# Kernel optimization log

Measured on AMD Instinct MI355X. Metric: run time of the kernel, lower is better.

Reference implementation:

```python
import jax, jax.numpy as jnp
import numpy as np
import math

N_NODES = 4096
NUM_FEATURES = 500
NHID = 256
RATIO = 0.75


def _build_adj(x):
    # Faithful vectorization of get_threshold/get_edge_index:
    # t = 0.5 * max_{i,j} ||x_i - x_j||^2 ; directed edges (src=i -> dst=j) for j>i with d2<t.
    # Dense adjacency A[dst, src] (jit-friendly; edge count is data-dependent in the original).
    sq = jnp.sum(x * x, axis=1)
    d2 = sq[:, None] + sq[None, :] - 2.0 * (x @ x.T)  # [N,N] squared distances
    t = 0.5 * jnp.max(d2)
    N = x.shape[0]
    lower = jnp.tril(jnp.ones((N, N), dtype=bool), k=-1)  # entry [j,i], j>i
    return jnp.where(lower & (d2 < t), 1.0, 0.0).astype(x.dtype)


def _gcn(A, x, W, b):
    # PyG GCNConv: add self-loops, symmetric normalization D^-1/2 (A+I) D^-1/2, then @ (xW) + b
    N = A.shape[0]
    Ah = A + jnp.eye(N, dtype=A.dtype)
    dis = jax.lax.rsqrt(jnp.sum(Ah, axis=1))  # deg >= 1 due to self loops
    norm = (dis[:, None] * Ah) * dis[None, :]
    return norm @ (x @ W) + b


def _sag_pool(A, x, Wr, Wn, bn, k):
    # SAGPooling with default GraphConv scorer: score = sum-aggr(neighbors)@Wn + bn + x@Wr
    score = jnp.tanh(((A @ x) @ Wn + bn + x @ Wr)[:, 0])  # [N]
    vals, perm = jax.lax.top_k(score, k)  # top ceil(ratio*N) nodes, descending
    xp = x[perm] * vals[:, None]
    Ap = A[perm][:, perm]  # filter edges to surviving nodes
    return Ap, xp


def _readout(x):
    # single graph (batch=None -> all zeros): [gmp, gap] -> [1, 2*nhid]
    return jnp.concatenate([jnp.max(x, axis=0), jnp.mean(x, axis=0)])[None, :]


def setup_inputs() -> dict:
    key = jax.random.key(0)
    ks = jax.random.split(key, 16)
    s = 0.02
    inp = {
        "feature": jax.random.normal(ks[0], (N_NODES, NUM_FEATURES), jnp.float32),
        "img_info": jax.random.normal(ks[1], (N_NODES, 6), jnp.float32),
        "W_pos": jax.random.normal(ks[2], (6, 12), jnp.float32) * s,
        "b_pos": jnp.zeros((12,), jnp.float32),
        "W1": jax.random.normal(ks[3], (512, NHID), jnp.float32) * s,
        "b1": jnp.zeros((NHID,), jnp.float32),
        "W2": jax.random.normal(ks[4], (NHID, NHID), jnp.float32) * s,
        "b2": jnp.zeros((NHID,), jnp.float32),
        "W3": jax.random.normal(ks[5], (NHID, NHID), jnp.float32) * s,
        "b3": jnp.zeros((NHID,), jnp.float32),
        "Wr1": jax.random.normal(ks[6], (NHID, 1), jnp.float32) * s,
        "Wn1": jax.random.normal(ks[7], (NHID, 1), jnp.float32) * s,
        "bs1": jnp.zeros((1,), jnp.float32),
        "Wr2": jax.random.normal(ks[8], (NHID, 1), jnp.float32) * s,
        "Wn2": jax.random.normal(ks[9], (NHID, 1), jnp.float32) * s,
        "bs2": jnp.zeros((1,), jnp.float32),
        "Wr3": jax.random.normal(ks[10], (NHID, 1), jnp.float32) * s,
        "Wn3": jax.random.normal(ks[11], (NHID, 1), jnp.float32) * s,
        "bs3": jnp.zeros((1,), jnp.float32),
    }
    return inp


def reference(feature, img_info, W_pos, b_pos, W1, b1, W2, b2, W3, b3,
              Wr1, Wn1, bs1, Wr2, Wn2, bs2, Wr3, Wn3, bs3):
    pos = jax.nn.relu(img_info @ W_pos + b_pos)          # [N,12]
    feat = jnp.concatenate([feature, pos], axis=1)       # [N,512]
    N = feat.shape[0]
    k1 = math.ceil(RATIO * N)
    k2 = math.ceil(RATIO * k1)
    k3 = math.ceil(RATIO * k2)

    A = _build_adj(feat)

    x = jax.nn.relu(_gcn(A, feat, W1, b1))
    A, x = _sag_pool(A, x, Wr1, Wn1, bs1, k1)
    x1 = _readout(x)

    x = jax.nn.relu(_gcn(A, x, W2, b2))
    A, x = _sag_pool(A, x, Wr2, Wn2, bs2, k2)
    x2 = _readout(x)

    x = jax.nn.relu(_gcn(A, x, W3, b3))
    A, x = _sag_pool(A, x, Wr3, Wn3, bs3, k3)
    x3 = _readout(x)

    return x1 + x2 + x3  # [1, 2*NHID]
```

## Files before the change

### kernel.cpp

```cpp
#include <hip/hip_runtime.h>
#include <hip/hip_bf16.h>
#include <math.h>

typedef __hip_bfloat16 bf16;
typedef unsigned short ushort;
typedef unsigned int uint;
typedef unsigned long long ull;
static __device__ __forceinline__ float b2f(bf16 x){ return __bfloat162float(x); }

static __device__ __forceinline__ float ldf(const void* p, int i, int isbf){
    return isbf ? b2f(((const bf16*)p)[i]) : ((const float*)p)[i];
}
static __device__ __forceinline__ ushort f2b(float x){
    return __bfloat16_as_ushort(__float2bfloat16(x));
}
static __device__ __forceinline__ uint fcode(float v){
    uint u = __float_as_uint(v);
    return (u & 0x80000000u) ? ~u : (u | 0x80000000u);
}
static __device__ __forceinline__ float fdecode(uint c){
    uint u = (c & 0x80000000u) ? (c & 0x7FFFFFFFu) : ~c;
    return __uint_as_float(u);
}

#define NN    4096
#define FEAT0 500
#define DIN   512
#define NH    256
#define KL1   3072
#define KL2   2304
#define KL3   1728
#define EDGE_CAP 786432u
#define NTRI  2080

typedef __attribute__((ext_vector_type(8)))  short v8s;
typedef __attribute__((ext_vector_type(16))) float v16f;

static __device__ __forceinline__ void gl_lds16(const ushort* g, ushort* l){
    __builtin_amdgcn_global_load_lds(
        (const __attribute__((address_space(1))) void*)g,
        (__attribute__((address_space(3))) void*)l, 16, 0, 0);
}

static __device__ __forceinline__ void detect_bf16(const void* p, int n, int t,
        uint* flag){
    if (t < 256 && t < n){
        uint e = ((uint)((const ushort*)p)[t] >> 7) & 0xFFu;
        if (e >= 135u) atomicAnd(flag, 0u);
    }
}

struct DtIn { const void* p[19]; int n[19]; };
__global__ __launch_bounds__(512) void k_prep(DtIn da,
        ushort* __restrict__ Xb, float* __restrict__ sq, ushort* __restrict__ Wb,
        unsigned* __restrict__ dflag, float* __restrict__ degA,
        uint* __restrict__ maxU, float* __restrict__ sums,
        unsigned* __restrict__ ecnt, unsigned* __restrict__ maxd2,
        float* __restrict__ tmin){
    int row = blockIdx.x, t = threadIdx.x;
    if (row < NN){
        __shared__ uint fl[4];
        if (t < 4) fl[t] = 1u;
        __syncthreads();
        detect_bf16(da.p[0], da.n[0], t, &fl[0]);
        detect_bf16(da.p[1], da.n[1], t, &fl[1]);
        detect_bf16(da.p[2], da.n[2], t, &fl[2]);
        detect_bf16(da.p[3], da.n[3], t, &fl[3]);
        __syncthreads();
        int f_feat = (int)fl[0], f_img = (int)fl[1], f_wp = (int)fl[2], f_bp = (int)fl[3];
        float v;
        if (t < FEAT0) v = ldf(da.p[0], row*FEAT0 + t, f_feat);
        else {
            int c = t - FEAT0;
            float acc = ldf(da.p[3], c, f_bp);
            #pragma unroll
            for (int d = 0; d < 6; d++)
                acc += ldf(da.p[1], row*6+d, f_img) * ldf(da.p[2], d*12+c, f_wp);
            v = fmaxf(acc, 0.f);
        }
        bf16 vb = __float2bfloat16(v);
        Xb[row*DIN + t] = __bfloat16_as_ushort(vb);
        float vr = b2f(vb);
        float vsq = vr*vr;
        #pragma unroll
        for (int off = 32; off >= 1; off >>= 1) vsq += __shfl_down(vsq, off);
        __shared__ float red[8];
        if ((t & 63) == 0) red[t >> 6] = vsq;
        __syncthreads();
        if (t == 0){
            float sres = 0.f;
            #pragma unroll
            for (int i = 0; i < 8; i++) sres += red[i];
            sq[row] = sres;
        }
    } else if (row < NN + 64){
        __shared__ uint fl[3];
        if (t < 3) fl[t] = 1u;
        __syncthreads();
        detect_bf16(da.p[4], da.n[4], t, &fl[0]);
        detect_bf16(da.p[6], da.n[6], t, &fl[1]);
        detect_bf16(da.p[8], da.n[8], t, &fl[2]);
        __syncthreads();
        int i0 = ((row - NN)*512 + t)*8;
        #pragma unroll
        for (int j = 0; j < 8; j++){
            int idx = i0 + j;
            float v;
            if (idx < 131072)       v = ldf(da.p[4], idx,          (int)fl[0]);
            else if (idx < 196608)  v = ldf(da.p[6], idx - 131072, (int)fl[1]);
            else                    v = ldf(da.p[8], idx - 196608, (int)fl[2]);
            Wb[idx] = __bfloat16_as_ushort(__float2bfloat16(v));
        }
    } else {
        __shared__ uint fl19[19];
        if (t < 19) fl19[t] = 1u;
        for (int i = t; i < NN; i += 512) degA[i] = 1.0f;
        for (int i = t; i < 4096; i += 512) tmin[i] = INFINITY;
        for (int i = t; i < 768; i += 512){ maxU[i] = 0x007FFFFFu; sums[i] = 0.f; }
        if (t == 0){
            #pragma unroll
            for (int i = 0; i < 8; i++) ecnt[i] = 0u;
            maxd2[0] = 0u;
        }
        __syncthreads();
        for (int idx = t; idx < 19*256; idx += 512){
            int i = idx >> 8, j = idx & 255;
            if (j < da.n[i]){
                uint e = ((uint)((const ushort*)da.p[i])[j] >> 7) & 0xFFu;
                if (e >= 135u) atomicAnd(&fl19[i], 0u);
            }
        }
        __syncthreads();
        if (t < 19) dflag[t] = fl19[t];
    }
}

static __device__ __forceinline__ v16f mm_tile(const ushort* __restrict__ Arows,
        const ushort* __restrict__ Brows, int K, ushort* As, ushort* Bs,
        int tid, int wv, int l31, int hi){
    int lane = tid & 63;
    int ro = lane >> 3, cch = lane & 7;
    int r0 = wv*16 + ro, r1 = wv*16 + 8 + ro;
    const ushort* gA0 = Arows + (size_t)r0*K + ((cch ^ (r0&7))<<3);
    const ushort* gA1 = Arows + (size_t)r1*K + ((cch ^ (r1&7))<<3);
    const ushort* gB0 = Brows + (size_t)r0*K + ((cch ^ (r0&7))<<3);
    const ushort* gB1 = Brows + (size_t)r1*K + ((cch ^ (r1&7))<<3);
    ushort* lA0 = As + (wv*16)*64;
    ushort* lA1 = As + (wv*16+8)*64;
    ushort* lB0 = Bs + (wv*16)*64;
    ushort* lB1 = Bs + (wv*16+8)*64;
    int wwr = wv >> 1, wwc = wv & 1;
    int ra0 = (wwr*32 + l31)*64, rbp = (wwc*32 + l31)*64;
    int fr7a = (wwr*32 + l31) & 7, fr7b = (wwc*32 + l31) & 7;
    v16f acc = {};
    int NC = K >> 6;
    for (int c = 0; c < NC; c++){
        int k0 = c*64;
        __syncthreads();
        gl_lds16(gA0 + k0, lA0);
        gl_lds16(gA1 + k0, lA1);
        gl_lds16(gB0 + k0, lB0);
        gl_lds16(gB1 + k0, lB1);
        __syncthreads();
        #pragma unroll
        for (int ks = 0; ks < 4; ks++){
            int gq = ks*2 + hi;
            v8s a = *(const v8s*)&As[ra0 + ((gq^fr7a)<<3)];
            v8s b = *(const v8s*)&Bs[rbp + ((gq^fr7b)<<3)];
            acc = __builtin_amdgcn_mfma_f32_32x32x16_bf16(a, b, acc, 0, 0, 0);
        }
    }
    return acc;
}

static __device__ __forceinline__ void xw_body(const ushort* __restrict__ Ab,
        const ushort* __restrict__ Wb, float* __restrict__ XW, int rb, int cb,
        int K, ushort* As, ushort* Bs){
    int tid = threadIdx.x, lane = tid & 63, wv = tid >> 6;
    int wwr = wv >> 1, wwc = wv & 1;
    int l31 = lane & 31, hi = lane >> 5;
    int arow0 = tid >> 3, ag = tid & 7;
    int arow1 = arow0 + 32;
    int da0 = arow0*64 + ((ag^(arow0&7))<<3);
    int da1 = arow1*64 + ((ag^(arow1&7))<<3);
    const size_t baseA = (size_t)rb*64*K;
    int kr = tid >> 2, ng = tid & 3;
    float4 a0p = *(const float4*)(Ab + baseA + (size_t)arow0*K + ag*8);
    float4 a1p = *(const float4*)(Ab + baseA + (size_t)arow1*K + ag*8);
    float4 b0p = *(const float4*)(Wb + (size_t)kr*NH + cb*64 + ng*16);
    float4 b1p = *(const float4*)(Wb + (size_t)kr*NH + cb*64 + ng*16 + 8);
    v16f acc = {};
    int ra0 = (wwr*32 + l31)*64, rbp = (wwc*32 + l31)*64;
    int fr7a = (wwr*32 + l31) & 7, fr7b = (wwc*32 + l31) & 7;
    int kg = kr >> 3, k7 = kr & 7;
    int NC = K >> 6;
    for (int c = 0; c < NC; c++){
        __syncthreads();
        *(float4*)&As[da0] = a0p; *(float4*)&As[da1] = a1p;
        const ushort* bw0 = (const ushort*)&b0p;
        const ushort* bw1 = (const ushort*)&b1p;
        #pragma unroll
        for (int j = 0; j < 8; j++){
            int nn = ng*16 + j;
            Bs[nn*64 + ((kg^(nn&7))<<3) + k7] = bw0[j];
        }
        #pragma unroll
        for (int j = 0; j < 8; j++){
            int nn = ng*16 + 8 + j;
            Bs[nn*64 + ((kg^(nn&7))<<3) + k7] = bw1[j];
        }
        __syncthreads();
        if (c + 1 < NC){
            int k0 = (c+1)*64;
            a0p = *(const float4*)(Ab + baseA + (size_t)arow0*K + k0 + ag*8);
            a1p = *(const float4*)(Ab + baseA + (size_t)arow1*K + k0 + ag*8);
            b0p = *(const float4*)(Wb + (size_t)(k0+kr)*NH + cb*64 + ng*16);
            b1p = *(const float4*)(Wb + (size_t)(k0+kr)*NH + cb*64 + ng*16 + 8);
        }
        #pragma unroll
        for (int ks = 0; ks < 4; ks++){
            int gq = ks*2 + hi;
            v8s a = *(const v8s*)&As[ra0 + ((gq^fr7a)<<3)];
            v8s b = *(const v8s*)&Bs[rbp + ((gq^fr7b)<<3)];
            acc = __builtin_amdgcn_mfma_f32_32x32x16_bf16(a, b, acc, 0, 0, 0);
        }
    }
    int n  = cb*64 + wwc*32 + l31;
    int mb = rb*64 + wwr*32 + 4*hi;
    #pragma unroll
    for (int i = 0; i < 16; i++){
        int m = mb + (i&3) + 8*(i>>2);
        XW[(size_t)m*NH + n] = acc[i];
    }
}

template<int PASS>
__global__ __launch_bounds__(256) void k_gram(const ushort* __restrict__ Xb,
        const float* __restrict__ sq, unsigned* __restrict__ maxd2,
        float* __restrict__ tmin, unsigned* __restrict__ ecnt,
        unsigned* __restrict__ edges, float* __restrict__ deg,
        const ushort* __restrict__ Wb, float* __restrict__ XW){
    __shared__ __align__(16) ushort As[64*64];
    __shared__ __align__(16) ushort Bs[64*64];
    int b = blockIdx.x;
    if (PASS == 1){
        if (b < 256){
            xw_body(Xb, Wb, XW, b >> 2, b & 3, DIN, As, Bs);
            return;
        }
        b -= 256;
    }
    float ff = sqrtf(8.f*(float)b + 1.f);
    int rb = (int)((ff - 1.f) * 0.5f);
    while ((rb+1)*(rb+2)/2 <= b) rb++;
    while (rb*(rb+1)/2 > b) rb--;
    int cb = b - rb*(rb+1)/2;

    int tid = threadIdx.x;
    float tthr = 0.f;
    if (PASS == 2){
        tthr = 0.5f * __uint_as_float(maxd2[0]);
        if (tmin[rb*64 + cb] >= tthr) return;
    }
    int lane = tid & 63, wv = tid >> 6;
    int l31 = lane & 31, hi = lane >> 5;
    int wwr = wv >> 1, wwc = wv & 1;
    v16f acc = mm_tile(Xb + (size_t)rb*64*DIN, Xb + (size_t)cb*64*DIN, DIN,
                       As, Bs, tid, wv, l31, hi);
    int rbase = rb*64 + wwr*32 + 4*hi;
    int col   = cb*64 + wwc*32 + l31;
    float sqc = sq[col];
    if (PASS == 1){
        float m = 0.f, mn = INFINITY;
        #pragma unroll
        for (int i = 0; i < 16; i++){
            int r = rbase + (i&3) + 8*(i>>2);
            float d2 = sq[r] + sqc - 2.f*acc[i];
            if (r != col) m = fmaxf(m, d2);
            if (r > col)  mn = fminf(mn, d2);
        }
        #pragma unroll
        for (int off = 32; off >= 1; off >>= 1){
            m  = fmaxf(m,  __shfl_down(m,  off));
            mn = fminf(mn, __shfl_down(mn, off));
        }
        __shared__ float wmax[4], wmin[4];
        if (lane == 0){ wmax[wv] = m; wmin[wv] = mn; }
        __syncthreads();
        if (tid == 0){
            float mm = fmaxf(fmaxf(wmax[0], wmax[1]), fmaxf(wmax[2], wmax[3]));
            tmin[rb*64 + cb] = fminf(fminf(wmin[0], wmin[1]), fminf(wmin[2], wmin[3]));
            atomicMax(maxd2, __float_as_uint(fmaxf(mm, 0.f)));
        }
    } else {
        #pragma unroll
        for (int i = 0; i < 16; i++){
            int r = rbase + (i&3) + 8*(i>>2);
            float d2 = sq[r] + sqc - 2.f*acc[i];
            if (r > col && d2 < tthr){
                unsigned idx = atomicAdd(ecnt, 1u);
                if (idx < EDGE_CAP){
                    edges[idx] = ((unsigned)r << 16) | (unsigned)col;
                    atomicAdd(&deg[r], 1.0f);
                }
            }
        }
    }
}

__global__ __launch_bounds__(256) void k_xwp(const float* __restrict__ Xn,
        const int* __restrict__ perm, const float* __restrict__ svals,
        const ushort* __restrict__ Wb, float* __restrict__ XW, int M,
        uint* __restrict__ maxU, float* __restrict__ sums, int layer){
    int rb = blockIdx.x, cb = blockIdx.y;
    __shared__ __align__(16) ushort As[64*64];
    __shared__ __align__(16) ushort Bs[64*64];
    __shared__ float pmx[256], psm[256];
    int tid = threadIdx.x, lane = tid & 63, wv = tid >> 6;
    int wwr = wv >> 1, wwc = wv & 1;
    int l31 = lane & 31, hi = lane >> 5;
    int arow0 = tid >> 3, ag = tid & 7;
    int arow1 = arow0 + 32;
    int da0 = arow0*64 + ((ag^(arow0&7))<<3);
    int da1 = arow1*64 + ((ag^(arow1&7))<<3);
    int p0 = perm[rb*64 + arow0]; float sv0 = svals[rb*64 + arow0];
    int p1 = perm[rb*64 + arow1]; float sv1 = svals[rb*64 + arow1];
    int kr = tid >> 2, ng = tid & 3;
    int kg = kr >> 3, k7 = kr & 7;
    int ra0 = (wwr*32 + l31)*64, rbp = (wwc*32 + l31)*64;
    int fr7a = (wwr*32 + l31) & 7, fr7b = (wwc*32 + l31) & 7;

    float4 xa0 = *(const float4*)(Xn + (size_t)p0*NH + ag*8);
    float4 xa1 = *(const float4*)(Xn + (size_t)p0*NH + ag*8 + 4);
    float4 xb0 = *(const float4*)(Xn + (size_t)p1*NH + ag*8);
    float4 xb1 = *(const float4*)(Xn + (size_t)p1*NH + ag*8 + 4);
    float4 wb0 = *(const float4*)(Wb + (size_t)kr*NH + cb*64 + ng*16);
    float4 wb1 = *(const float4*)(Wb + (size_t)kr*NH + cb*64 + ng*16 + 8);

    v16f acc = {};
    for (int c = 0; c < 4; c++){
        __syncthreads();
        {
            __align__(16) ushort ta[8];
            ta[0]=f2b(xa0.x*sv0); ta[1]=f2b(xa0.y*sv0); ta[2]=f2b(xa0.z*sv0); ta[3]=f2b(xa0.w*sv0);
            ta[4]=f2b(xa1.x*sv0); ta[5]=f2b(xa1.y*sv0); ta[6]=f2b(xa1.z*sv0); ta[7]=f2b(xa1.w*sv0);
            *(float4*)&As[da0] = *(const float4*)ta;
            __align__(16) ushort tb[8];
            tb[0]=f2b(xb0.x*sv1); tb[1]=f2b(xb0.y*sv1); tb[2]=f2b(xb0.z*sv1); tb[3]=f2b(xb0.w*sv1);
            tb[4]=f2b(xb1.x*sv1); tb[5]=f2b(xb1.y*sv1); tb[6]=f2b(xb1.z*sv1); tb[7]=f2b(xb1.w*sv1);
            *(float4*)&As[da1] = *(const float4*)tb;
        }
        {
            const ushort* bw0 = (const ushort*)&wb0;
            const ushort* bw1 = (const ushort*)&wb1;
            #pragma unroll
            for (int j = 0; j < 8; j++){
                int nn = ng*16 + j;
                Bs[nn*64 + ((kg^(nn&7))<<3) + k7] = bw0[j];
            }
            #pragma unroll
            for (int j = 0; j < 8; j++){
                int nn = ng*16 + 8 + j;
                Bs[nn*64 + ((kg^(nn&7))<<3) + k7] = bw1[j];
            }
        }
        __syncthreads();
        if (c < 3){
            int k0 = (c+1)*64;
            xa0 = *(const float4*)(Xn + (size_t)p0*NH + k0 + ag*8);
            xa1 = *(const float4*)(Xn + (size_t)p0*NH + k0 + ag*8 + 4);
            xb0 = *(const float4*)(Xn + (size_t)p1*NH + k0 + ag*8);
            xb1 = *(const float4*)(Xn + (size_t)p1*NH + k0 + ag*8 + 4);
            wb0 = *(const float4*)(Wb + (size_t)(k0+kr)*NH + cb*64 + ng*16);
            wb1 = *(const float4*)(Wb + (size_t)(k0+kr)*NH + cb*64 + ng*16 + 8);
        }
        if (cb == 0){
            int cc = tid & 63, q = tid >> 6;
            int gg = cc >> 3, c7 = cc & 7;
            float m = -INFINITY, s = 0.f;
            #pragma unroll
            for (int i = 0; i < 16; i++){
                int rr = q*16 + i;
                float v = __uint_as_float(((uint)As[rr*64 + ((gg^(rr&7))<<3) + c7]) << 16);
                m = fmaxf(m, v); s += v;
            }
            pmx[tid] = m; psm[tid] = s;
            __syncthreads();
            if (tid < 64){
                float mm = fmaxf(fmaxf(pmx[tid], pmx[tid+64]), fmaxf(pmx[tid+128], pmx[tid+192]));
                float ss = psm[tid] + psm[tid+64] + psm[tid+128] + psm[tid+192];
                atomicMax(&maxU[layer*NH + c*64 + tid], fcode(mm));
                atomicAdd(&sums[layer*NH + c*64 + tid], ss);
            }
        }
        #pragma unroll
        for (int ks = 0; ks < 4; ks++){
            int gq = ks*2 + hi;
            v8s a = *(const v8s*)&As[ra0 + ((gq^fr7a)<<3)];
            v8s b = *(const v8s*)&Bs[rbp + ((gq^fr7b)<<3)];
            acc = __builtin_amdgcn_mfma_f32_32x32x16_bf16(a, b, acc, 0, 0, 0);
        }
    }
    int n  = cb*64 + wwc*32 + l31;
    int mb = rb*64 + wwr*32 + 4*hi;
    #pragma unroll
    for (int i = 0; i < 16; i++){
        int m = mb + (i&3) + 8*(i>>2);
        XW[(size_t)m*NH + n] = acc[i];
    }
}

__global__ __launch_bounds__(256) void k_gcnscore(const float* __restrict__ XW,
        const unsigned* __restrict__ edges, const unsigned* __restrict__ ecnt, int slot,
        const float* __restrict__ deg, const void* __restrict__ b,
        const void* __restrict__ Wn, const void* __restrict__ Wr, const void* __restrict__ bs,
        const unsigned* __restrict__ fb, const unsigned* __restrict__ fWn,
        const unsigned* __restrict__ fWr, const unsigned* __restrict__ fbs,
        float* __restrict__ Xn, float* __restrict__ s1, float* __restrict__ z){
    int row = blockIdx.x, t = threadIdx.x;
    __shared__ unsigned eL[256];
    __shared__ unsigned Esh;
    if (t == 0){ unsigned E0 = ecnt[slot]; Esh = (E0 > EDGE_CAP) ? EDGE_CAP : E0; }
    __syncthreads();
    unsigned E = Esh;
    float disr = 1.0f / sqrtf(deg[row]);
    float acc = disr * XW[row*NH + t];
    for (unsigned base = 0; base < E; base += 256){
        unsigned nchunk = E - base; if (nchunk > 256) nchunk = 256;
        __syncthreads();
        if (t < nchunk) eL[t] = edges[base + t];
        __syncthreads();
        for (unsigned j = 0; j < nchunk; j++){
            unsigned ed = eL[j];
            if ((int)(ed >> 16) == row){
                int src = ed & 0xFFFFu;
                acc += (1.0f / sqrtf(deg[src])) * XW[src*NH + t];
            }
        }
    }
    float xn = fmaxf(fmaf(disr, acc, ldf(b, t, (int)fb[0])), 0.f);
    Xn[row*NH + t] = xn;
    float a  = xn * ldf(Wn, t, (int)fWn[0]);
    float bb = xn * ldf(Wr, t, (int)fWr[0]);
    for (int off = 32; off >= 1; off >>= 1){ a += __shfl_down(a, off); bb += __shfl_down(bb, off); }
    __shared__ float ra[4], rbv[4];
    int w = t >> 6;
    if ((t & 63) == 0){ ra[w] = a; rbv[w] = bb; }
    __syncthreads();
    if (t == 0){
        s1[row] = ra[0]+ra[1]+ra[2]+ra[3];
        z[row]  = rbv[0]+rbv[1]+rbv[2]+rbv[3] + ldf(bs, 0, (int)fbs[0]);
    }
}

static __device__ __forceinline__ uint2 radix_scan(const uint* hist, uint* wt,
        uint* ws, uint* sh, int t, int lane, int wv, uint kk, int NB){
    uint loc = 0;
    int b0 = t << 2;
    if (b0 < NB) loc = hist[b0] + hist[b0+1] + hist[b0+2] + hist[b0+3];
    uint s = loc;
    #pragma unroll
    for (int off = 1; off < 64; off <<= 1){
        uint u = __shfl_down(s, off);
        if (lane + off < 64) s += u;
    }
    if (lane == 0) wt[wv] = s;
    __syncthreads();
    if (t < 16){
        uint a = 0;
        for (int j = t + 1; j < 16; j++) a += wt[j];
        ws[t] = a;
    }
    __syncthreads();
    if (b0 < NB){
        uint run = ws[wv] + (s - loc);
        for (int b = b0 + 3; b >= b0; b--){
            uint h = hist[b];
            if (run < kk && run + h >= kk){ sh[0] = (uint)b; sh[1] = run; }
            run += h;
        }
    }
    __syncthreads();
    return make_uint2(sh[0], sh[1]);
}

__global__ __launch_bounds__(1024) void k_select(const float* __restrict__ z,
        const float* __restrict__ s1, int N, int k,
        const unsigned* __restrict__ eIn, unsigned* __restrict__ ecnt, int slotCur,
        unsigned* __restrict__ eOut, int slotOut,
        int* __restrict__ perm, float* __restrict__ svals,
        float* __restrict__ degN, int Nnext){
    __shared__ float zsh[4096];
    __shared__ int   rnk[4096];
    __shared__ uint  hist[4096];
    __shared__ uint  wcnt[16];
    __shared__ uint  wbase[16];
    __shared__ uint  sh[4];
    int t = threadIdx.x;
    int lane = t & 63, wv = t >> 6;
    for (int i = t; i < N; i += 1024){ zsh[i] = z[i]; rnk[i] = -1; }
    for (int i = t; i < Nnext; i += 1024) degN[i] = 1.0f;
    if (t == 0) sh[2] = 0u;
    __syncthreads();
    unsigned E = ecnt[slotCur]; if (E > EDGE_CAP) E = EDGE_CAP;
    for (unsigned e = t; e < E; e += 1024){
        unsigned ed = eIn[e];
        atomicAdd(&zsh[ed >> 16], s1[ed & 0xFFFFu]);
    }
    __syncthreads();
    bool v0 = t < N,        v1 = t+1024 < N,  v2 = t+2048 < N,  v3 = t+3072 < N;
    uint c0 = v0 ? fcode(zsh[t])      : 0u;
    uint c1 = v1 ? fcode(zsh[t+1024]) : 0u;
    uint c2 = v2 ? fcode(zsh[t+2048]) : 0u;
    uint c3 = v3 ? fcode(zsh[t+3072]) : 0u;

    for (int i = t; i < 4096; i += 1024) hist[i] = 0u;
    __syncthreads();
    if (v0){
        uint h0 = c0 >> 20, h1 = c1 >> 20, h2 = c2 >> 20, h3 = c3 >> 20;
        bool u1 = v1, u2 = v2, u3 = v3;
        uint n0 = 1;
        if (u1 && h1 == h0){ n0++; u1 = false; }
        if (u2 && h2 == h0){ n0++; u2 = false; }
        if (u3 && h3 == h0){ n0++; u3 = false; }
        atomicAdd(&hist[h0], n0);
        if (u1){
            uint n1 = 1;
            if (u2 && h2 == h1){ n1++; u2 = false; }
            if (u3 && h3 == h1){ n1++; u3 = false; }
            atomicAdd(&hist[h1], n1);
        }
        if (u2){
            uint n2 = 1;
            if (u3 && h3 == h2){ n2++; u3 = false; }
            atomicAdd(&hist[h2], n2);
        }
        if (u3) atomicAdd(&hist[h3], 1u);
    }
    __syncthreads();
    uint2 p1 = radix_scan(hist, wcnt, wbase, sh, t, lane, wv, (uint)k, 4096);
    uint B1 = p1.x; uint kk2 = (uint)k - p1.y;
    for (int i = t; i < 4096; i += 1024) hist[i] = 0u;
    __syncthreads();
    if (v0 && (c0 >> 20) == B1) atomicAdd(&hist[(c0 >> 8) & 0xFFFu], 1u);
    if (v1 && (c1 >> 20) == B1) atomicAdd(&hist[(c1 >> 8) & 0xFFFu], 1u);
    if (v2 && (c2 >> 20) == B1) atomicAdd(&hist[(c2 >> 8) & 0xFFFu], 1u);
    if (v3 && (c3 >> 20) == B1) atomicAdd(&hist[(c3 >> 8) & 0xFFFu], 1u);
    __syncthreads();
    uint2 p2 = radix_scan(hist, wcnt, wbase, sh, t, lane, wv, kk2, 4096);
    uint B2 = p2.x; uint kk3 = kk2 - p2.y;
    uint hi24 = (B1 << 12) | B2;
    for (int i = t; i < 256; i += 1024) hist[i] = 0u;
    __syncthreads();
    if (v0 && (c0 >> 8) == hi24) atomicAdd(&hist[c0 & 0xFFu], 1u);
    if (v1 && (c1 >> 8) == hi24) atomicAdd(&hist[c1 & 0xFFu], 1u);
    if (v2 && (c2 >> 8) == hi24) atomicAdd(&hist[c2 & 0xFFu], 1u);
    if (v3 && (c3 >> 8) == hi24) atomicAdd(&hist[c3 & 0xFFu], 1u);
    __syncthreads();
    uint2 p3 = radix_scan(hist, wcnt, wbase, sh, t, lane, wv, kk3, 256);
    uint T = (B1 << 20) | (B2 << 8) | p3.x;

    ull b0 = __ballot(v0 && c0 > T), b1 = __ballot(v1 && c1 > T);
    ull b2 = __ballot(v2 && c2 > T), b3 = __ballot(v3 && c3 > T);
    uint t0 = (uint)__popcll(b0), t1 = (uint)__popcll(b1);
    uint t2 = (uint)__popcll(b2), t3 = (uint)__popcll(b3);
    if (lane == 0) wcnt[wv] = t0 + t1 + t2 + t3;
    __syncthreads();
    if (t == 0){
        uint s = 0;
        for (int i = 0; i < 16; i++){ wbase[i] = s; s += wcnt[i]; }
        sh[1] = s;
    }
    __syncthreads();
    uint cntGT = sh[1];
    uint rem = (uint)k - cntGT;
    ull ltm = ((ull)1 << lane) - 1;
    uint off = wbase[wv];
    if (v0 && c0 > T){ uint r = off + (uint)__popcll(b0 & ltm); int i = t;
        perm[r] = i; svals[r] = tanhf(zsh[i]); rnk[i] = (int)r; }
    off += t0;
    if (v1 && c1 > T){ uint r = off + (uint)__popcll(b1 & ltm); int i = t+1024;
        perm[r] = i; svals[r] = tanhf(zsh[i]); rnk[i] = (int)r; }
    off += t1;
    if (v2 && c2 > T){ uint r = off + (uint)__popcll(b2 & ltm); int i = t+2048;
        perm[r] = i; svals[r] = tanhf(zsh[i]); rnk[i] = (int)r; }
    off += t2;
    if (v3 && c3 > T){ uint r = off + (uint)__popcll(b3 & ltm); int i = t+3072;
        perm[r] = i; svals[r] = tanhf(zsh[i]); rnk[i] = (int)r; }
    #pragma unroll
    for (int j = 0; j < 4; j++){
        int i = t + j*1024;
        bool vv = (j==0) ? v0 : (j==1) ? v1 : (j==2) ? v2 : v3;
        uint cc = (j==0) ? c0 : (j==1) ? c1 : (j==2) ? c2 : c3;
        if (vv && cc == T){
            uint e = atomicAdd(&sh[2], 1u);
            if (e < rem){
                uint r = cntGT + e;
                perm[r] = i; svals[r] = tanhf(zsh[i]); rnk[i] = (int)r;
            }
        }
    }
    __syncthreads();
    if (slotOut >= 0){
        for (unsigned e = t; e < E; e += 1024){
            unsigned ed = eIn[e];
            int nd = rnk[ed >> 16], ns = rnk[ed & 0xFFFFu];
            if (nd >= 0 && ns >= 0){
                unsigned idx = atomicAdd(&ecnt[slotOut], 1u);
                if (idx < EDGE_CAP){
                    eOut[idx] = ((unsigned)nd << 16) | (unsigned)ns;
                    atomicAdd(&degN[nd], 1.0f);
                }
            }
        }
    }
}

__global__ __launch_bounds__(256) void k_poolread3(const float* __restrict__ Xn,
        const int* __restrict__ perm, const float* __restrict__ svals, int k,
        uint* __restrict__ maxU, float* __restrict__ sums,
        unsigned* __restrict__ done, float* __restrict__ out){
    int b = blockIdx.x, t = threadIdx.x;
    float m = -INFINITY, s = 0.f;
    for (int r = b; r < k; r += 64){
        int p = perm[r];
        float v = Xn[p*NH + t] * svals[r];
        m = fmaxf(m, v); s += v;
    }
    atomicMax(&maxU[2*NH + t], fcode(m));
    atomicAdd(&sums[2*NH + t], s);
    __threadfence();
    __shared__ uint lastv;
    if (t == 0) lastv = atomicAdd(done, 1u);
    __syncthreads();
    if (lastv == 63u){
        uint m0 = atomicAdd(&maxU[t], 0u);
        uint m1 = atomicAdd(&maxU[NH + t], 0u);
        uint m2 = atomicAdd(&maxU[2*NH + t], 0u);
        float s0 = atomicAdd(&sums[t], 0.f);
        float s1v = atomicAdd(&sums[NH + t], 0.f);
        float s2 = atomicAdd(&sums[2*NH + t], 0.f);
        out[t] = fdecode(m0) + fdecode(m1) + fdecode(m2);
        out[NH + t] = s0*(1.0f/KL1) + s1v*(1.0f/KL2) + s2*(1.0f/KL3);
    }
}

extern "C" void kernel_launch(void* const* d_in, const int* in_sizes, int n_in,
                              void* d_out, int out_size, void* d_ws, size_t ws_size,
                              hipStream_t stream)
{
    const void* b1 = d_in[5];
    const void* b2 = d_in[7];
    const void* b3 = d_in[9];
    const void* Wr1 = d_in[10]; const void* Wn1 = d_in[11]; const void* bs1 = d_in[12];
    const void* Wr2 = d_in[13]; const void* Wn2 = d_in[14]; const void* bs2 = d_in[15];
    const void* Wr3 = d_in[16]; const void* Wn3 = d_in[17]; const void* bs3 = d_in[18];

    char* w = (char*)d_ws;
    auto alloc = [&](size_t bytes)->char*{ char* p = w; w += (bytes + 255) & ~(size_t)255; return p; };
    ushort*   Xb    = (ushort*)  alloc((size_t)NN*DIN*2);
    float*    Xn    = (float*)   alloc((size_t)NN*NH*4);
    float*    XW    = (float*)   alloc((size_t)NN*NH*4);
    ushort*   Wb    = (ushort*)  alloc((size_t)262144*2);
    unsigned* E0    = (unsigned*)alloc((size_t)EDGE_CAP*4);
    unsigned* E1    = (unsigned*)alloc((size_t)EDGE_CAP*4);
    float*    tmin  = (float*)   alloc(4096*4);
    float*    sq    = (float*)   alloc(NN*4);
    float*    degA  = (float*)   alloc(NN*4);
    float*    degB  = (float*)   alloc(NN*4);
    float*    s1    = (float*)   alloc(NN*4);
    float*    z     = (float*)   alloc(NN*4);
    int*      perm  = (int*)     alloc(NN*4);
    float*    svals = (float*)   alloc(NN*4);
    unsigned* ecnt  = (unsigned*)alloc(256);
    unsigned* maxd2 = (unsigned*)alloc(256);
    unsigned* dflag = (unsigned*)alloc(256);
    uint*     maxU  = (uint*)    alloc(768*4);
    float*    sums  = (float*)   alloc(768*4);
    (void)ws_size;

    DtIn da;
    for (int i = 0; i < 19; i++){ da.p[i] = d_in[i]; da.n[i] = in_sizes[i]; }

    k_prep<<<NN + 65, 512, 0, stream>>>(da, Xb, sq, Wb, dflag, degA, maxU, sums,
            ecnt, maxd2, tmin);
    k_gram<1><<<256 + NTRI, 256, 0, stream>>>(Xb, sq, maxd2, tmin, ecnt, E0, degA,
            Wb, XW);
    k_gram<2><<<NTRI, 256, 0, stream>>>(Xb, sq, maxd2, tmin, ecnt, E0, degA,
            Wb, XW);

    k_gcnscore<<<NN, 256, 0, stream>>>(XW, E0, ecnt, 0, degA, b1, Wn1, Wr1, bs1,
            dflag+5, dflag+11, dflag+10, dflag+12, Xn, s1, z);
    k_select<<<1, 1024, 0, stream>>>(z, s1, NN, KL1, E0, ecnt, 0, E1, 1,
            perm, svals, degB, KL1);

    k_xwp<<<dim3(48,4), 256, 0, stream>>>(Xn, perm, svals, Wb + 131072, XW, KL1,
            maxU, sums, 0);
    k_gcnscore<<<KL1, 256, 0, stream>>>(XW, E1, ecnt, 1, degB, b2, Wn2, Wr2, bs2,
            dflag+7, dflag+14, dflag+13, dflag+15, Xn, s1, z);
    k_select<<<1, 1024, 0, stream>>>(z, s1, KL1, KL2, E1, ecnt, 1, E0, 2,
            perm, svals, degA, KL2);

    k_xwp<<<dim3(36,4), 256, 0, stream>>>(Xn, perm, svals, Wb + 196608, XW, KL2,
            maxU, sums, 1);
    k_gcnscore<<<KL2, 256, 0, stream>>>(XW, E0, ecnt, 2, degA, b3, Wn3, Wr3, bs3,
            dflag+9, dflag+17, dflag+16, dflag+18, Xn, s1, z);
    k_select<<<1, 1024, 0, stream>>>(z, s1, KL2, KL3, E0, ecnt, 2,
            (unsigned*)nullptr, -1, perm, svals, degB, 0);
    k_poolread3<<<64, 256, 0, stream>>>(Xn, perm, svals, KL3, maxU, sums,
            ecnt + 3, (float*)d_out);
}
```

Before: 231.5 us.

## Enlarge Gram-matrix tiles to 128x128 with 512-thread blocks

The pairwise-distance Gram kernels now use 128x128 triangular tiles computed by 8 waves, each doing two MFMA accumulators that share one A fragment. This replaces 64x64 tiles. The fused XW part also moves to 128-row blocks and loads A through direct global-to-LDS loads. The goal is to cut redundant global/LDS traffic per output and the block count. In exchange, the coarser tile-skip in pass 2 prunes less, and the fewer, larger blocks may reduce occupancy.

```diff
diff --git a/kernel.cpp b/kernel.cpp
--- a/kernel.cpp
+++ b/kernel.cpp
@@ -31,7 +31,7 @@
 #define KL2   2304
 #define KL3   1728
 #define EDGE_CAP 786432u
-#define NTRI  2080
+#define NT128 528
 
 typedef __attribute__((ext_vector_type(8)))  short v8s;
 typedef __attribute__((ext_vector_type(16))) float v16f;
@@ -42,6 +42,7 @@
         (__attribute__((address_space(3))) void*)l, 16, 0, 0);
 }
 
+struct DtIn { const void* p[19]; int n[19]; };
 static __device__ __forceinline__ void detect_bf16(const void* p, int n, int t,
         uint* flag){
     if (t < 256 && t < n){
@@ -49,8 +50,6 @@
         if (e >= 135u) atomicAnd(flag, 0u);
     }
 }
-
-struct DtIn { const void* p[19]; int n[19]; };
 __global__ __launch_bounds__(512) void k_prep(DtIn da,
         ushort* __restrict__ Xb, float* __restrict__ sq, ushort* __restrict__ Wb,
         unsigned* __restrict__ dflag, float* __restrict__ degA,
@@ -135,26 +134,30 @@
     }
 }
 
-static __device__ __forceinline__ v16f mm_tile(const ushort* __restrict__ Arows,
-        const ushort* __restrict__ Brows, int K, ushort* As, ushort* Bs,
-        int tid, int wv, int l31, int hi){
-    int lane = tid & 63;
+struct A2 { v16f a0; v16f a1; };
+static __device__ __forceinline__ A2 mm_tile128(const ushort* __restrict__ Arows,
+        const ushort* __restrict__ Brows, ushort* As, ushort* Bs, int tid){
+    int lane = tid & 63, wv = tid >> 6;
+    int l31 = lane & 31, hi = lane >> 5;
     int ro = lane >> 3, cch = lane & 7;
     int r0 = wv*16 + ro, r1 = wv*16 + 8 + ro;
-    const ushort* gA0 = Arows + (size_t)r0*K + ((cch ^ (r0&7))<<3);
-    const ushort* gA1 = Arows + (size_t)r1*K + ((cch ^ (r1&7))<<3);
-    const ushort* gB0 = Brows + (size_t)r0*K + ((cch ^ (r0&7))<<3);
-    const ushort* gB1 = Brows + (size_t)r1*K + ((cch ^ (r1&7))<<3);
+    const ushort* gA0 = Arows + (size_t)r0*DIN + ((cch ^ (r0&7))<<3);
+    const ushort* gA1 = Arows + (size_t)r1*DIN + ((cch ^ (r1&7))<<3);
+    const ushort* gB0 = Brows + (size_t)r0*DIN + ((cch ^ (r0&7))<<3);
+    const ushort* gB1 = Brows + (size_t)r1*DIN + ((cch ^ (r1&7))<<3);
     ushort* lA0 = As + (wv*16)*64;
     ushort* lA1 = As + (wv*16+8)*64;
     ushort* lB0 = Bs + (wv*16)*64;
     ushort* lB1 = Bs + (wv*16+8)*64;
-    int wwr = wv >> 1, wwc = wv & 1;
-    int ra0 = (wwr*32 + l31)*64, rbp = (wwc*32 + l31)*64;
-    int fr7a = (wwr*32 + l31) & 7, fr7b = (wwc*32 + l31) & 7;
-    v16f acc = {};
-    int NC = K >> 6;
-    for (int c = 0; c < NC; c++){
+    int wr = wv >> 1, wc = wv & 1;
+    int ar = wr*32 + l31;
+    int br0 = wc*64 + l31;
+    int br1 = wc*64 + 32 + l31;
+    int ra  = ar*64,  f7a = ar & 7;
+    int rb0 = br0*64, f7b0 = br0 & 7;
+    int rb1 = br1*64, f7b1 = br1 & 7;
+    v16f acc0 = {}, acc1 = {};
+    for (int c = 0; c < DIN/64; c++){
         int k0 = c*64;
         __syncthreads();
         gl_lds16(gA0 + k0, lA0);
@@ -165,68 +168,63 @@
         #pragma unroll
         for (int ks = 0; ks < 4; ks++){
             int gq = ks*2 + hi;
-            v8s a = *(const v8s*)&As[ra0 + ((gq^fr7a)<<3)];
-            v8s b = *(const v8s*)&Bs[rbp + ((gq^fr7b)<<3)];
-            acc = __builtin_amdgcn_mfma_f32_32x32x16_bf16(a, b, acc, 0, 0, 0);
-        }
-    }
-    return acc;
-}
-
-static __device__ __forceinline__ void xw_body(const ushort* __restrict__ Ab,
+            v8s a  = *(const v8s*)&As[ra  + ((gq^f7a )<<3)];
+            v8s b0 = *(const v8s*)&Bs[rb0 + ((gq^f7b0)<<3)];
+            v8s b1 = *(const v8s*)&Bs[rb1 + ((gq^f7b1)<<3)];
+            acc0 = __builtin_amdgcn_mfma_f32_32x32x16_bf16(a, b0, acc0, 0, 0, 0);
+            acc1 = __builtin_amdgcn_mfma_f32_32x32x16_bf16(a, b1, acc1, 0, 0, 0);
+        }
+    }
+    A2 r; r.a0 = acc0; r.a1 = acc1;
+    return r;
+}
+
+static __device__ __forceinline__ void xw_body128(const ushort* __restrict__ Ab,
         const ushort* __restrict__ Wb, float* __restrict__ XW, int rb, int cb,
-        int K, ushort* As, ushort* Bs){
+        ushort* As, ushort* Bs){
     int tid = threadIdx.x, lane = tid & 63, wv = tid >> 6;
-    int wwr = wv >> 1, wwc = wv & 1;
     int l31 = lane & 31, hi = lane >> 5;
-    int arow0 = tid >> 3, ag = tid & 7;
-    int arow1 = arow0 + 32;
-    int da0 = arow0*64 + ((ag^(arow0&7))<<3);
-    int da1 = arow1*64 + ((ag^(arow1&7))<<3);
-    const size_t baseA = (size_t)rb*64*K;
-    int kr = tid >> 2, ng = tid & 3;
-    float4 a0p = *(const float4*)(Ab + baseA + (size_t)arow0*K + ag*8);
-    float4 a1p = *(const float4*)(Ab + baseA + (size_t)arow1*K + ag*8);
-    float4 b0p = *(const float4*)(Wb + (size_t)kr*NH + cb*64 + ng*16);
-    float4 b1p = *(const float4*)(Wb + (size_t)kr*NH + cb*64 + ng*16 + 8);
+    int ro = lane >> 3, cch = lane & 7;
+    int r0 = wv*16 + ro, r1 = wv*16 + 8 + ro;
+    const ushort* Arows = Ab + (size_t)rb*128*DIN;
+    const ushort* gA0 = Arows + (size_t)r0*DIN + ((cch ^ (r0&7))<<3);
+    const ushort* gA1 = Arows + (size_t)r1*DIN + ((cch ^ (r1&7))<<3);
+    ushort* lA0 = As + (wv*16)*64;
+    ushort* lA1 = As + (wv*16+8)*64;
+    int kr = tid >> 3, ch = tid & 7;
+    int kg = kr >> 3, k7 = kr & 7;
+    float4 wv4 = *(const float4*)(Wb + (size_t)kr*NH + cb*64 + ch*8);
+    int wr = wv >> 1, wc = wv & 1;
+    int ar = wr*32 + l31;
+    int brr = wc*32 + l31;
+    int ra = ar*64,  f7a = ar & 7;
+    int rbp = brr*64, f7b = brr & 7;
     v16f acc = {};
-    int ra0 = (wwr*32 + l31)*64, rbp = (wwc*32 + l31)*64;
-    int fr7a = (wwr*32 + l31) & 7, fr7b = (wwc*32 + l31) & 7;
-    int kg = kr >> 3, k7 = kr & 7;
-    int NC = K >> 6;
-    for (int c = 0; c < NC; c++){
-        __syncthreads();
-        *(float4*)&As[da0] = a0p; *(float4*)&As[da1] = a1p;
-        const ushort* bw0 = (const ushort*)&b0p;
-        const ushort* bw1 = (const ushort*)&b1p;
-        #pragma unroll
-        for (int j = 0; j < 8; j++){
-            int nn = ng*16 + j;
-            Bs[nn*64 + ((kg^(nn&7))<<3) + k7] = bw0[j];
-        }
-        #pragma unroll
-        for (int j = 0; j < 8; j++){
-            int nn = ng*16 + 8 + j;
-            Bs[nn*64 + ((kg^(nn&7))<<3) + k7] = bw1[j];
-        }
-        __syncthreads();
-        if (c + 1 < NC){
-            int k0 = (c+1)*64;
-            a0p = *(const float4*)(Ab + baseA + (size_t)arow0*K + k0 + ag*8);
-            a1p = *(const float4*)(Ab + baseA + (size_t)arow1*K + k0 + ag*8);
-            b0p = *(const float4*)(Wb + (size_t)(k0+kr)*NH + cb*64 + ng*16);
-            b1p = *(const float4*)(Wb + (size_t)(k0+kr)*NH + cb*64 + ng*16 + 8);
-        }
+    for (int c = 0; c < DIN/64; c++){
+        __syncthreads();
+        gl_lds16(gA0 + c*64, lA0);
+        gl_lds16(gA1 + c*64, lA1);
+        {
+            const ushort* ws = (const ushort*)&wv4;
+            #pragma unroll
+            for (int j = 0; j < 8; j++){
+                int nn = ch*8 + j;
+                Bs[nn*64 + ((kg^(nn&7))<<3) + k7] = ws[j];
+            }
+        }
+        __syncthreads();
+        if (c + 1 < DIN/64)
+            wv4 = *(const float4*)(Wb + (size_t)((c+1)*64+kr)*NH + cb*64 + ch*8);
         #pragma unroll
         for (int ks = 0; ks < 4; ks++){
             int gq = ks*2 + hi;
-            v8s a = *(const v8s*)&As[ra0 + ((gq^fr7a)<<3)];
-            v8s b = *(const v8s*)&Bs[rbp + ((gq^fr7b)<<3)];
+            v8s a = *(const v8s*)&As[ra  + ((gq^f7a)<<3)];
+            v8s b = *(const v8s*)&Bs[rbp + ((gq^f7b)<<3)];
             acc = __builtin_amdgcn_mfma_f32_32x32x16_bf16(a, b, acc, 0, 0, 0);
         }
     }
-    int n  = cb*64 + wwc*32 + l31;
-    int mb = rb*64 + wwr*32 + 4*hi;
+    int n  = cb*64 + wc*32 + l31;
+    int mb = rb*128 + wr*32 + 4*hi;
     #pragma unroll
     for (int i = 0; i < 16; i++){
         int m = mb + (i&3) + 8*(i>>2);
@@ -235,20 +233,20 @@
 }
 
 template<int PASS>
-__global__ __launch_bounds__(256) void k_gram(const ushort* __restrict__ Xb,
+__global__ __launch_bounds__(512, 4) void k_gram(const ushort* __restrict__ Xb,
         const float* __restrict__ sq, unsigned* __restrict__ maxd2,
         float* __restrict__ tmin, unsigned* __restrict__ ecnt,
         unsigned* __restrict__ edges, float* __restrict__ deg,
         const ushort* __restrict__ Wb, float* __restrict__ XW){
-    __shared__ __align__(16) ushort As[64*64];
-    __shared__ __align__(16) ushort Bs[64*64];
+    __shared__ __align__(16) ushort As[128*64];
+    __shared__ __align__(16) ushort Bs[128*64];
     int b = blockIdx.x;
     if (PASS == 1){
-        if (b < 256){
-            xw_body(Xb, Wb, XW, b >> 2, b & 3, DIN, As, Bs);
+        if (b < 128){
+            xw_body128(Xb, Wb, XW, b >> 2, b & 3, As, Bs);
             return;
         }
-        b -= 256;
+        b -= 128;
     }
     float ff = sqrtf(8.f*(float)b + 1.f);
     int rb = (int)((ff - 1.f) * 0.5f);
@@ -260,47 +258,63 @@
     float tthr = 0.f;
     if (PASS == 2){
         tthr = 0.5f * __uint_as_float(maxd2[0]);
-        if (tmin[rb*64 + cb] >= tthr) return;
+        if (tmin[rb*32 + cb] >= tthr) return;
     }
     int lane = tid & 63, wv = tid >> 6;
     int l31 = lane & 31, hi = lane >> 5;
-    int wwr = wv >> 1, wwc = wv & 1;
-    v16f acc = mm_tile(Xb + (size_t)rb*64*DIN, Xb + (size_t)cb*64*DIN, DIN,
-                       As, Bs, tid, wv, l31, hi);
-    int rbase = rb*64 + wwr*32 + 4*hi;
-    int col   = cb*64 + wwc*32 + l31;
-    float sqc = sq[col];
+    int wr = wv >> 1, wc = wv & 1;
+    A2 acc = mm_tile128(Xb + (size_t)rb*128*DIN, Xb + (size_t)cb*128*DIN,
+                        As, Bs, tid);
+    int rbase = rb*128 + wr*32 + 4*hi;
+    int col0  = cb*128 + wc*64 + l31;
+    int col1  = col0 + 32;
+    float sqc0 = sq[col0], sqc1 = sq[col1];
     if (PASS == 1){
         float m = 0.f, mn = INFINITY;
         #pragma unroll
         for (int i = 0; i < 16; i++){
             int r = rbase + (i&3) + 8*(i>>2);
-            float d2 = sq[r] + sqc - 2.f*acc[i];
-            if (r != col) m = fmaxf(m, d2);
-            if (r > col)  mn = fminf(mn, d2);
+            float d20 = sq[r] + sqc0 - 2.f*acc.a0[i];
+            float d21 = sq[r] + sqc1 - 2.f*acc.a1[i];
+            if (r != col0) m = fmaxf(m, d20);
+            if (r >  col0) mn = fminf(mn, d20);
+            if (r != col1) m = fmaxf(m, d21);
+            if (r >  col1) mn = fminf(mn, d21);
         }
         #pragma unroll
         for (int off = 32; off >= 1; off >>= 1){
             m  = fmaxf(m,  __shfl_down(m,  off));
             mn = fminf(mn, __shfl_down(mn, off));
         }
-        __shared__ float wmax[4], wmin[4];
+        __shared__ float wmax[8], wmin[8];
         if (lane == 0){ wmax[wv] = m; wmin[wv] = mn; }
         __syncthreads();
         if (tid == 0){
-            float mm = fmaxf(fmaxf(wmax[0], wmax[1]), fmaxf(wmax[2], wmax[3]));
-            tmin[rb*64 + cb] = fminf(fminf(wmin[0], wmin[1]), fminf(wmin[2], wmin[3]));
+            float mm = wmax[0], mmn = wmin[0];
+            #pragma unroll
+            for (int i = 1; i < 8; i++){
+                mm = fmaxf(mm, wmax[i]); mmn = fminf(mmn, wmin[i]);
+            }
+            tmin[rb*32 + cb] = mmn;
             atomicMax(maxd2, __float_as_uint(fmaxf(mm, 0.f)));
         }
     } else {
         #pragma unroll
         for (int i = 0; i < 16; i++){
             int r = rbase + (i&3) + 8*(i>>2);
-            float d2 = sq[r] + sqc - 2.f*acc[i];
-            if (r > col && d2 < tthr){
+            float d20 = sq[r] + sqc0 - 2.f*acc.a0[i];
+            if (r > col0 && d20 < tthr){
                 unsigned idx = atomicAdd(ecnt, 1u);
                 if (idx < EDGE_CAP){
-                    edges[idx] = ((unsigned)r << 16) | (unsigned)col;
+                    edges[idx] = ((unsigned)r << 16) | (unsigned)col0;
+                    atomicAdd(&deg[r], 1.0f);
+                }
+            }
+            float d21 = sq[r] + sqc1 - 2.f*acc.a1[i];
+            if (r > col1 && d21 < tthr){
+                unsigned idx = atomicAdd(ecnt, 1u);
+                if (idx < EDGE_CAP){
+                    edges[idx] = ((unsigned)r << 16) | (unsigned)col1;
                     atomicAdd(&deg[r], 1.0f);
                 }
             }
@@ -684,9 +698,9 @@
 
     k_prep<<<NN + 65, 512, 0, stream>>>(da, Xb, sq, Wb, dflag, degA, maxU, sums,
             ecnt, maxd2, tmin);
-    k_gram<1><<<256 + NTRI, 256, 0, stream>>>(Xb, sq, maxd2, tmin, ecnt, E0, degA,
+    k_gram<1><<<128 + NT128, 512, 0, stream>>>(Xb, sq, maxd2, tmin, ecnt, E0, degA,
             Wb, XW);
-    k_gram<2><<<NTRI, 256, 0, stream>>>(Xb, sq, maxd2, tmin, ecnt, E0, degA,
+    k_gram<2><<<NT128, 512, 0, stream>>>(Xb, sq, maxd2, tmin, ecnt, E0, degA,
             Wb, XW);
 
     k_gcnscore<<<NN, 256, 0, stream>>>(XW, E0, ecnt, 0, degA, b1, Wn1, Wr1, bs1,
```

New measurement: 213.0 us, median of 2. 8.0% less time.
